# Optimization experiments

Hardware: AMD Instinct MI355X
Metric: run time of the kernel (lower is better)

The kernel has to match this reference:

```python
import jax, jax.numpy as jnp
import numpy as np

K = 1.0          # Lorentz curvature param: x_t^2 - |x_s|^2 = K
SQRT_K = 1.0
EPS = 1e-8
HEADS = 12

def add_time(s):
    t = jnp.sqrt(K + jnp.sum(s * s, axis=-1, keepdims=True))
    return jnp.concatenate([t, s], axis=-1)

def lorentz_ln(x, g, b):
    s = x[..., 1:]
    mu = jnp.mean(s, axis=-1, keepdims=True)
    var = jnp.var(s, axis=-1, keepdims=True)
    s = (s - mu) / jnp.sqrt(var + 1e-5) * g + b
    return add_time(s)

def lorentz_fc(x, W, heads=None, act=None):
    # linear on full Lorentz vector -> space part; time recomputed to stay on manifold
    s = x @ W.T
    if act is not None:
        s = act(s)
    if heads is not None:
        bsz, n, dt = s.shape
        s = s.reshape(bsz, n, heads, dt // heads).transpose(0, 2, 1, 3)  # (b,h,n,hd)
    return add_time(s)

def logmap0(x):
    t, s = x[..., :1], x[..., 1:]
    sn = jnp.sqrt(jnp.sum(s * s, axis=-1, keepdims=True))
    dist = SQRT_K * jnp.arccosh(jnp.maximum(t / SQRT_K, 1.0 + 1e-7))
    u = dist * s / jnp.maximum(sn, EPS)
    return jnp.concatenate([jnp.zeros_like(t), u], axis=-1)

def expmap0(u):
    us = u[..., 1:]
    n = jnp.sqrt(jnp.sum(us * us, axis=-1, keepdims=True))
    nc = jnp.maximum(n, EPS)
    t = SQRT_K * jnp.cosh(n / SQRT_K)
    s = SQRT_K * jnp.sinh(n / SQRT_K) * us / nc
    return jnp.concatenate([t, s], axis=-1)

def ste_clip(x, lo, hi):
    # straight-through estimator: clamp in fwd, identity grad
    return x + jax.lax.stop_gradient(jnp.clip(x, lo, hi) - x)

def ste_max_clamp(x, hi):
    return x + jax.lax.stop_gradient(jnp.minimum(x, hi) - x)

def mha_last_layer(x, Wq, Wk, Wv, Wo, alpha_raw, tau_raw, lambda_raw):
    q = lorentz_fc(x, Wq, heads=HEADS)   # (b,h,n,hd+1)
    k = lorentz_fc(x, Wk, heads=HEADS)
    v = lorentz_fc(x, Wv, heads=HEADS)
    q_t, q_s = q[..., :1], q[..., 1:]
    k_t, k_s = k[..., :1], k[..., 1:]
    # Lorentzian inner product -> hyperbolic pairwise distances
    inner_QK = -q_t @ jnp.swapaxes(k_t, -1, -2) + jnp.einsum('bhid,bhjd->bhij', q_s, k_s)
    raw_cosh = jnp.maximum(-inner_QK / K, 1.0)                # (b,h,n,n)
    is_self = raw_cosh < 1.0 + 1e-5
    safe_cosh = jnp.where(is_self, 2.0, raw_cosh)
    dist_QK = SQRT_K * jnp.arccosh(safe_cosh)
    cosh_OQ = jnp.maximum(q_t / SQRT_K, 1.0 + 1e-7)
    cosh_OK = jnp.maximum(k_t / SQRT_K, 1.0 + 1e-7)
    c_tilde = jnp.minimum(SQRT_K * jnp.arccosh(cosh_OQ), 40.0) / SQRT_K  # (b,h,n,1)
    sinh_QK = jnp.sinh(dist_QK / SQRT_K)
    sinh_OQ = jnp.sinh(c_tilde)
    numer = raw_cosh * cosh_OQ - jnp.swapaxes(cosh_OK, -1, -2)
    raw_Z = numer / (sinh_OQ * sinh_QK)
    Z_safe = jnp.where(is_self, 1.0, ste_clip(raw_Z, -1.0, 1.0))
    alpha = jax.nn.softplus(alpha_raw)
    B = alpha * c_tilde / (1.0 + alpha * c_tilde)
    lam = jax.nn.softplus(lambda_raw)
    d_L = ste_max_clamp(dist_QK, 40.0)   # float32 branch of STE_Dist_Clamp
    log_dist_penalty = -lam * jnp.log1p(d_L * d_L)
    m = 0.1
    entail = jax.nn.softplus(B + Z_safe - m) - jax.nn.softplus(jnp.asarray(-m, B.dtype))
    tau = jax.nn.softplus(tau_raw)
    score = jax.nn.softmax(log_dist_penalty - tau * entail, axis=-1)
    # expmap aggregation: tangent-space weighted mean
    v_tan = logmap0(v)
    agg = jnp.einsum('bhij,bhjd->bhid', score, v_tan)
    agg = agg / (jnp.sum(score, axis=-1, keepdims=True) + 1e-8)
    attn = expmap0(agg).transpose(0, 2, 1, 3)   # (b,n,h,hd+1)
    bsz, n, h, _ = attn.shape
    attn_s = attn[..., 1:].reshape(bsz, n, -1)
    attn_t = attn[..., :1].reshape(bsz, n, -1)
    t_new = jnp.sqrt(jnp.sum(attn_t ** 2, axis=-1, keepdims=True) - (h - 1) * K)
    return lorentz_fc(jnp.concatenate([t_new, attn_s], axis=-1), Wo)


def setup_inputs() -> dict:
    key = jax.random.key(0)
    ks = jax.random.split(key, 8)
    b, n, hidden, mlp_hidden = 4, 1024, 769, 3073
    d = hidden - 1
    xs = jax.random.normal(ks[0], (b, n, d), jnp.float32)
    x = add_time(xs)
    def w(k, o, i):
        return jax.random.normal(k, (o, i), jnp.float32) * (i ** -0.5)
    return {
        'x': x,
        'Wq': w(ks[1], d, hidden), 'Wk': w(ks[2], d, hidden), 'Wv': w(ks[3], d, hidden),
        'Wo': w(ks[4], d, hidden),
        'ln1_g': jnp.ones((d,), jnp.float32), 'ln1_b': jnp.zeros((d,), jnp.float32),
        'ln2_g': jnp.ones((d,), jnp.float32), 'ln2_b': jnp.zeros((d,), jnp.float32),
        'Wm1': w(ks[5], mlp_hidden - 1, hidden), 'Wm2': w(ks[6], d, mlp_hidden),
        'alpha_raw': jnp.zeros((1,), jnp.float32),
        'tau_raw': jnp.zeros((1,), jnp.float32),
        'lambda_raw': jnp.zeros((1,), jnp.float32),
    }


def reference(x, Wq, Wk, Wv, Wo, ln1_g, ln1_b, ln2_g, ln2_b, Wm1, Wm2, alpha_raw, tau_raw, lambda_raw):
    out = mha_last_layer(lorentz_ln(x, ln1_g, ln1_b), Wq, Wk, Wv, Wo, alpha_raw, tau_raw, lambda_raw)
    out = out[..., 1:] + x[..., 1:]                 # residual on space part (DropPath=identity in eval)
    h = lorentz_ln(add_time(out), ln2_g, ln2_b)
    h = lorentz_fc(h, Wm1, act=lambda z: jax.nn.gelu(z, approximate=False))
    h = lorentz_fc(h, Wm2)
    out = h[..., 1:] + out
    return add_time(out)
```

## Files before the change

kernel.cpp:

```cpp
#include <hip/hip_runtime.h>
#include <cstdint>
#include <cstddef>

typedef unsigned short u16;
typedef __attribute__((ext_vector_type(8))) __bf16 bf16x8;
typedef __attribute__((ext_vector_type(4))) float f32x4;

#define SEQ 1024
#define MROWS 4096
#define DDIM 768
#define HID 769
#define KP1 800
#define MLPD 3072
#define KP2 3104
#define NHEADS 12
#define LN2F 0.69314718056f
#define LOG2EF 1.44269504089f

static __device__ __forceinline__ u16 f2bf(float f){
  union { float f; uint32_t u; } v; v.f = f;
  return (u16)((v.u + 0x7FFFu + ((v.u >> 16) & 1u)) >> 16);
}

static __device__ __forceinline__ f32x4 mfma16(bf16x8 a, bf16x8 b, f32x4 c){
  return __builtin_amdgcn_mfma_f32_16x16x32_bf16(a, b, c, 0, 0, 0);
}

static __device__ __forceinline__ void async_lds16(const u16* g, u16* l){
  u16* gm = const_cast<u16*>(g);
  __builtin_amdgcn_global_load_lds(
      (__attribute__((address_space(1))) void*)gm,
      (__attribute__((address_space(3))) void*)l, 16, 0, 0);
}

static __device__ __forceinline__ float blk_reduce(float v, float* red, int tid){
  #pragma unroll
  for (int off = 1; off < 64; off <<= 1) v += __shfl_xor(v, off, 64);
  __syncthreads();
  if ((tid & 63) == 0) red[tid >> 6] = v;
  __syncthreads();
  return red[0] + red[1] + red[2] + red[3];
}

static __device__ __forceinline__ void conv_seg(const float* W, u16* O, int idx, int K, int Kp){
  int n = idx / Kp, k = idx - n * Kp;
  O[idx] = (k < K) ? f2bf(W[(size_t)n * K + k]) : (u16)0;
}
__global__ __launch_bounds__(256) void conv_all(const float* __restrict__ Wq, const float* __restrict__ Wk,
    const float* __restrict__ Wv, const float* __restrict__ Wo,
    const float* __restrict__ Wm1, const float* __restrict__ Wm2, u16* __restrict__ dst){
  int b = blockIdx.x, tid = threadIdx.x;
  if (b < 2400){        conv_seg(Wq,  dst,            b*256+tid,        769, 800); }
  else if (b < 4800){   conv_seg(Wk,  dst + 614400,  (b-2400)*256+tid,  769, 800); }
  else if (b < 7200){   conv_seg(Wv,  dst + 1228800, (b-4800)*256+tid,  769, 800); }
  else if (b < 9600){   conv_seg(Wo,  dst + 1843200, (b-7200)*256+tid,  769, 800); }
  else if (b < 19200){  conv_seg(Wm1, dst + 2457600, (b-9600)*256+tid,  769, 800); }
  else {                conv_seg(Wm2, dst + 4915200, (b-19200)*256+tid, 3073, 3104); }
}

__global__ __launch_bounds__(256) void ln_kernel(const float* __restrict__ X, int xstr, int xoff,
    const float* __restrict__ g, const float* __restrict__ b, u16* __restrict__ O){
  __shared__ float red[4];
  int m = blockIdx.x, tid = threadIdx.x;
  const float* xr = X + (size_t)m * xstr + xoff;
  float s[3], y[3];
  float s1 = 0.f, s2 = 0.f;
  #pragma unroll
  for (int j = 0; j < 3; j++){ float v = xr[tid + j*256]; s[j] = v; s1 += v; s2 += v*v; }
  s1 = blk_reduce(s1, red, tid);
  s2 = blk_reduce(s2, red, tid);
  float mu = s1 * (1.f/768.f);
  float var = s2 * (1.f/768.f) - mu*mu;
  float rstd = rsqrtf(var + 1e-5f);
  float q = 0.f;
  #pragma unroll
  for (int j = 0; j < 3; j++){ int i = tid + j*256; y[j] = (s[j]-mu)*rstd*g[i] + b[i]; q += y[j]*y[j]; }
  q = blk_reduce(q, red, tid);
  u16* orow = O + (size_t)m * KP1;
  #pragma unroll
  for (int j = 0; j < 3; j++) orow[1 + tid + j*256] = f2bf(y[j]);
  if (tid == 0) orow[0] = f2bf(sqrtf(1.f + q));
  if (tid < 31) orow[769 + tid] = 0;
}

__global__ __launch_bounds__(256) void ln_sum_kernel(const float* __restrict__ P4,
    const float* __restrict__ x, const float* __restrict__ g, const float* __restrict__ b,
    float* __restrict__ out1, u16* __restrict__ O){
  __shared__ float red[4];
  int m = blockIdx.x, tid = threadIdx.x;
  float s[3], y[3];
  float s1 = 0.f, s2 = 0.f;
  #pragma unroll
  for (int j = 0; j < 3; j++){
    int col = tid + j*256;
    float v = x[(size_t)m * HID + 1 + col];
    #pragma unroll
    for (int z = 0; z < 4; z++) v += P4[(size_t)z*MROWS*DDIM + (size_t)m*DDIM + col];
    out1[(size_t)m*DDIM + col] = v;
    s[j] = v; s1 += v; s2 += v*v;
  }
  s1 = blk_reduce(s1, red, tid);
  s2 = blk_reduce(s2, red, tid);
  float mu = s1 * (1.f/768.f);
  float var = s2 * (1.f/768.f) - mu*mu;
  float rstd = rsqrtf(var + 1e-5f);
  float q = 0.f;
  #pragma unroll
  for (int j = 0; j < 3; j++){ int i = tid + j*256; y[j] = (s[j]-mu)*rstd*g[i] + b[i]; q += y[j]*y[j]; }
  q = blk_reduce(q, red, tid);
  u16* orow = O + (size_t)m * KP1;
  #pragma unroll
  for (int j = 0; j < 3; j++) orow[1 + tid + j*256] = f2bf(y[j]);
  if (tid == 0) orow[0] = f2bf(sqrtf(1.f + q));
  if (tid < 31) orow[769 + tid] = 0;
}

__global__ __launch_bounds__(256) void gemm_qkv(
    const u16* __restrict__ A,
    const u16* __restrict__ B0, const u16* __restrict__ B1, const u16* __restrict__ B2,
    float* __restrict__ C, int N, int Kp)
{
  __shared__ u16 As[128*32];
  __shared__ u16 Bs[128*32];
  int tid = threadIdx.x;
  int wave = tid >> 6, lane = tid & 63;
  int lrow = lane & 15, lq = lane >> 4;
  int m0 = blockIdx.y * 128, n0 = blockIdx.x * 128;
  int wm = wave >> 1, wn = wave & 1;
  const u16* B = (blockIdx.z == 0) ? B0 : (blockIdx.z == 1 ? B1 : B2);
  C += (size_t)blockIdx.z * MROWS * N;
  f32x4 acc[4][4] = {};
  int seg = wave * 2;
  int srow = lane >> 2;
  int scol = (lane & 3) * 8;
  const u16* Abase = A + (size_t)m0 * Kp;
  const u16* Bbase = B + (size_t)n0 * Kp;
  for (int k0 = 0; k0 < Kp; k0 += 32){
    __syncthreads();
    #pragma unroll
    for (int i = 0; i < 2; i++){
      int s = seg + i;
      async_lds16(Abase + (size_t)(s*16 + srow) * Kp + k0 + scol, As + s*512);
      async_lds16(Bbase + (size_t)(s*16 + srow) * Kp + k0 + scol, Bs + s*512);
    }
    __syncthreads();
    bf16x8 af[4], bfr[4];
    #pragma unroll
    for (int t = 0; t < 4; t++){
      af[t]  = *(const bf16x8*)(As + (wm*64 + t*16 + lrow)*32 + lq*8);
      bfr[t] = *(const bf16x8*)(Bs + (wn*64 + t*16 + lrow)*32 + lq*8);
    }
    #pragma unroll
    for (int mt = 0; mt < 4; mt++)
      #pragma unroll
      for (int nt = 0; nt < 4; nt++)
        acc[mt][nt] = mfma16(af[mt], bfr[nt], acc[mt][nt]);
  }
  #pragma unroll
  for (int mt = 0; mt < 4; mt++)
    #pragma unroll
    for (int nt = 0; nt < 4; nt++){
      int col = n0 + wn*64 + nt*16 + lrow;
      #pragma unroll
      for (int r = 0; r < 4; r++){
        int row = m0 + wm*64 + mt*16 + lq*4 + r;
        C[(size_t)row * N + col] = acc[mt][nt][r];
      }
    }
}

__global__ __launch_bounds__(256) void gemm_split(
    const u16* __restrict__ A, const u16* __restrict__ B, float* __restrict__ C,
    int N, int Kp)
{
  __shared__ u16 As[128*32];
  __shared__ u16 Bs[128*32];
  int tid = threadIdx.x;
  int wave = tid >> 6, lane = tid & 63;
  int lrow = lane & 15, lq = lane >> 4;
  int m0 = blockIdx.y * 128, n0 = blockIdx.x * 128;
  int wm = wave >> 1, wn = wave & 1;
  int chunks = Kp >> 5;
  int nz = gridDim.z, z = blockIdx.z;
  int base = chunks / nz, rem = chunks - base * nz;
  int begin = z * base + (z < rem ? z : rem);
  int count = base + (z < rem ? 1 : 0);
  C += (size_t)z * MROWS * N;
  f32x4 acc[4][4] = {};
  int seg = wave * 2;
  int srow = lane >> 2;
  int scol = (lane & 3) * 8;
  const u16* Abase = A + (size_t)m0 * Kp;
  const u16* Bbase = B + (size_t)n0 * Kp;
  for (int kc = begin; kc < begin + count; kc++){
    int k0 = kc * 32;
    __syncthreads();
    #pragma unroll
    for (int i = 0; i < 2; i++){
      int s = seg + i;
      async_lds16(Abase + (size_t)(s*16 + srow) * Kp + k0 + scol, As + s*512);
      async_lds16(Bbase + (size_t)(s*16 + srow) * Kp + k0 + scol, Bs + s*512);
    }
    __syncthreads();
    bf16x8 af[4], bfr[4];
    #pragma unroll
    for (int t = 0; t < 4; t++){
      af[t]  = *(const bf16x8*)(As + (wm*64 + t*16 + lrow)*32 + lq*8);
      bfr[t] = *(const bf16x8*)(Bs + (wn*64 + t*16 + lrow)*32 + lq*8);
    }
    #pragma unroll
    for (int mt = 0; mt < 4; mt++)
      #pragma unroll
      for (int nt = 0; nt < 4; nt++)
        acc[mt][nt] = mfma16(af[mt], bfr[nt], acc[mt][nt]);
  }
  #pragma unroll
  for (int mt = 0; mt < 4; mt++)
    #pragma unroll
    for (int nt = 0; nt < 4; nt++){
      int col = n0 + wn*64 + nt*16 + lrow;
      #pragma unroll
      for (int r = 0; r < 4; r++){
        int row = m0 + wm*64 + mt*16 + lq*4 + r;
        C[(size_t)row * N + col] = acc[mt][nt][r];
      }
    }
}

__global__ __launch_bounds__(256) void pack_qk(const float* __restrict__ raw,
    u16* __restrict__ Qp, u16* __restrict__ Kpk, float* __restrict__ qt, float* __restrict__ kt)
{
  int wave = threadIdx.x >> 6, lane = threadIdx.x & 63;
  int m = blockIdx.x * 4 + wave;
  int h = blockIdx.y;
  int which = blockIdx.z;
  const float* src = raw + (size_t)which * MROWS * DDIM + (size_t)m * DDIM + h*64 + lane;
  float v = *src;
  float ss = v*v;
  #pragma unroll
  for (int off = 1; off < 64; off <<= 1) ss += __shfl_xor(ss, off, 64);
  int b = m >> 10, n = m & 1023, bh = b * NHEADS + h;
  u16* dst = (which ? Kpk : Qp) + ((size_t)bh * SEQ + n) * 64 + lane;
  *dst = f2bf(v);
  if (lane == 0) (which ? kt : qt)[bh * SEQ + n] = sqrtf(1.f + ss);
}

__global__ __launch_bounds__(256) void pack_v(const float* __restrict__ vraw, u16* __restrict__ Vt){
  __shared__ float part[256];
  __shared__ float scl[64];
  __shared__ float tile[64][65];
  int tid = threadIdx.x;
  int kb = blockIdx.x, bh = blockIdx.y;
  int b = bh / NHEADS, h = bh - b*NHEADS;
  int kl = tid >> 2;
  int d0 = (tid & 3) * 16;
  int m = b * SEQ + kb * 64 + kl;
  float v[16]; float ss = 0.f;
  const float* src = vraw + (size_t)m * DDIM + h*64 + d0;
  #pragma unroll
  for (int i = 0; i < 16; i++){ v[i] = src[i]; ss += v[i]*v[i]; }
  part[tid] = ss;
  __syncthreads();
  if ((tid & 3) == 0){
    float s2 = part[tid] + part[tid+1] + part[tid+2] + part[tid+3];
    float sn = sqrtf(s2);
    float tv = sqrtf(1.f + s2);
    float ctv = fmaxf(tv, 1.f + 1e-7f);
    float dist = __logf(ctv + sqrtf(fmaxf(ctv*ctv - 1.f, 0.f)));
    scl[kl] = dist / fmaxf(sn, 1e-8f);
  }
  __syncthreads();
  float sc = scl[kl];
  #pragma unroll
  for (int i = 0; i < 16; i++) tile[kl][d0 + i] = v[i] * sc;
  __syncthreads();
  int dim = tid >> 2;
  int kk0 = (tid & 3) * 16;
  u16 tmp[16];
  #pragma unroll
  for (int i = 0; i < 16; i++) tmp[i] = f2bf(tile[kk0 + i][dim]);
  u16* dst = Vt + ((size_t)bh * 64 + dim) * SEQ + kb*64 + kk0;
  *(uint4*)dst       = *(const uint4*)tmp;
  *(uint4*)(dst + 8) = *(const uint4*)(tmp + 8);
}

__global__ __launch_bounds__(256) void attn_kernel(
    const u16* __restrict__ Q, const u16* __restrict__ K, const u16* __restrict__ Vt,
    const float* __restrict__ qt, const float* __restrict__ kt,
    float* __restrict__ pAgg, float* __restrict__ pDen,
    const float* __restrict__ a_raw, const float* __restrict__ t_raw, const float* __restrict__ l_raw)
{
  __shared__ float rv[4][64];
  __shared__ u16 Pl[4][16*72];
  int tid = threadIdx.x;
  int bh = blockIdx.y, ks = blockIdx.z;
  int qbase = blockIdx.x * 64;
  float alpha = __logf(1.f + __expf(a_raw[0]));
  float tau   = __logf(1.f + __expf(t_raw[0]));
  float lam   = __logf(1.f + __expf(l_raw[0]));
  if (tid < 64){
    float qtv = qt[bh * SEQ + qbase + tid];
    float cq = fmaxf(qtv, 1.f + 1e-7f);
    float A = cq + __builtin_amdgcn_sqrtf(fmaxf(cq*cq - 1.f, 0.f));
    float ct = fminf(__builtin_amdgcn_logf(A) * LN2F, 40.f);
    float e = __expf(ct);
    float sh = 0.5f * (e - __builtin_amdgcn_rcpf(e));
    float ac = alpha * ct;
    rv[0][tid] = qtv;
    rv[1][tid] = cq;
    rv[2][tid] = __builtin_amdgcn_rcpf(sh);
    rv[3][tid] = (ac * __builtin_amdgcn_rcpf(1.f + ac) - 0.1f) * LOG2EF;
  }
  __syncthreads();
  int wave = tid >> 6, lane = tid & 63;
  int lrow = lane & 15, lq = lane >> 4;
  int myrow = wave*16 + lrow;
  float qt_l = rv[0][myrow], cq_l = rv[1][myrow], rri_l = rv[2][myrow], Bw_l = rv[3][myrow];
  const float tbase = tau * 0.92967051f;
  const u16* Qb = Q + ((size_t)bh * SEQ + qbase + wave*16 + lrow) * 64 + lq*8;
  bf16x8 bq0 = *(const bf16x8*)Qb;
  bf16x8 bq1 = *(const bf16x8*)(Qb + 32);
  const u16* Kh = K + (size_t)bh * SEQ * 64;
  const u16* Vh = Vt + (size_t)bh * 64 * SEQ;
  const float* ktp = kt + (size_t)bh * SEQ;
  u16* Pw = &Pl[wave][0];
  f32x4 o[4] = {};
  float dsum = 0.f;
  for (int jt = 0; jt < 8; jt++){
    int jbase = ks * 512 + jt * 64;
    f32x4 s[4];
    #pragma unroll
    for (int ct = 0; ct < 4; ct++){
      const u16* Ka = Kh + (size_t)(jbase + ct*16 + lrow) * 64 + lq*8;
      bf16x8 a0 = *(const bf16x8*)Ka;
      bf16x8 a1 = *(const bf16x8*)(Ka + 32);
      f32x4 z = {0.f, 0.f, 0.f, 0.f};
      z = mfma16(a0, bq0, z);
      z = mfma16(a1, bq1, z);
      s[ct] = z;
    }
    #pragma unroll
    for (int ct = 0; ct < 4; ct++){
      float4 kv = *(const float4*)(ktp + jbase + ct*16 + lq*4);
      uint32_t pu[4];
      #pragma unroll
      for (int r = 0; r < 4; r++){
        float ktv = (r == 0) ? kv.x : (r == 1) ? kv.y : (r == 2) ? kv.z : kv.w;
        float c = fmaxf(__builtin_fmaf(qt_l, ktv, -s[ct][r]), 1.f);
        bool self = c < 1.00001f;
        float ce = self ? 2.f : c;
        float cm1 = __builtin_fmaf(ce, ce, -1.f);
        float rs = __builtin_amdgcn_rsqf(cm1);
        float shq = cm1 * rs;
        float d = fminf(__builtin_amdgcn_logf(ce + shq) * LN2F, 40.f);
        float L1 = __builtin_amdgcn_logf(__builtin_fmaf(d, d, 1.f));
        float Z = __builtin_fmaf(ce, cq_l, -ktv) * rri_l * rs;
        Z = fminf(fmaxf(Z, -1.f), 1.f);
        Z = self ? 1.f : Z;
        float w2 = __builtin_fmaf(Z, LOG2EF, Bw_l);
        float ew = __builtin_amdgcn_exp2f(w2);
        float L2 = __builtin_amdgcn_logf(ew + 1.f);
        float logit = __builtin_fmaf(-lam, L1, __builtin_fmaf(-tau, L2, tbase));
        float p = __builtin_amdgcn_exp2f(logit);
        uint32_t u = __float_as_uint(p);
        pu[r] = u;
        dsum += __uint_as_float(u & 0xFFFF0000u);
      }
      uint32_t lo = __builtin_amdgcn_perm(pu[1], pu[0], 0x07060302u);
      uint32_t hi = __builtin_amdgcn_perm(pu[3], pu[2], 0x07060302u);
      uint2 pk; pk.x = lo; pk.y = hi;
      *(uint2*)(Pw + lrow*72 + ct*16 + lq*4) = pk;
    }
    bf16x8 ap0 = *(const bf16x8*)(Pw + lrow*72 + lq*8);
    bf16x8 ap1 = *(const bf16x8*)(Pw + lrow*72 + 32 + lq*8);
    #pragma unroll
    for (int nt = 0; nt < 4; nt++){
      const u16* Vb = Vh + (size_t)(nt*16 + lrow) * SEQ + jbase + lq*8;
      bf16x8 bv0 = *(const bf16x8*)Vb;
      bf16x8 bv1 = *(const bf16x8*)(Vb + 32);
      o[nt] = mfma16(ap0, bv0, o[nt]);
      o[nt] = mfma16(ap1, bv1, o[nt]);
    }
  }
  dsum += __shfl_xor(dsum, 16, 64);
  dsum += __shfl_xor(dsum, 32, 64);
  size_t pbase = ((size_t)(ks*48 + bh) * SEQ) + qbase;
  if (lq == 0) pDen[pbase + wave*16 + lrow] = dsum;
  #pragma unroll
  for (int nt = 0; nt < 4; nt++)
    #pragma unroll
    for (int r = 0; r < 4; r++)
      pAgg[(pbase + wave*16 + lq*4 + r) * 64 + nt*16 + lrow] = o[nt][r];
}

__global__ __launch_bounds__(768) void expmap_pack(const float* __restrict__ pAgg,
    const float* __restrict__ pDen, u16* __restrict__ O){
  __shared__ float th2[NHEADS];
  int m = blockIdx.x, tid = threadIdx.x;
  int h = tid >> 6, lane = tid & 63;
  int b = m >> 10, n = m & 1023, bh = b*NHEADS + h;
  size_t i0 = ((size_t)bh * SEQ + n);
  size_t i1 = ((size_t)(48 + bh) * SEQ + n);
  float d = pDen[i0] + pDen[i1];
  float rden = __builtin_amdgcn_rcpf(d * (1.f + 1e-8f));
  float u = (pAgg[i0*64 + lane] + pAgg[i1*64 + lane]) * rden;
  float n2 = u*u;
  #pragma unroll
  for (int off = 1; off < 64; off <<= 1) n2 += __shfl_xor(n2, off, 64);
  float nn = sqrtf(n2);
  float e = __expf(nn);
  float ch = 0.5f * (e + 1.f/e);
  float sh = 0.5f * (e - 1.f/e);
  float sc = sh / fmaxf(nn, 1e-8f);
  u16* orow = O + (size_t)m * KP1;
  orow[1 + h*64 + lane] = f2bf(u * sc);
  if (lane == 0) th2[h] = ch*ch;
  __syncthreads();
  if (tid == 0){
    float ssum = 0.f;
    #pragma unroll
    for (int i = 0; i < NHEADS; i++) ssum += th2[i];
    orow[0] = f2bf(sqrtf(ssum - 11.f));
  }
  if (tid >= 1 && tid < 32) orow[768 + tid] = 0;
}

__global__ __launch_bounds__(256) void gelu_pack(const float* __restrict__ Zin, u16* __restrict__ O){
  __shared__ float red[4];
  int m = blockIdx.x, tid = threadIdx.x;
  const float* zr = Zin + (size_t)m * MLPD;
  float gv[12]; float gs = 0.f;
  #pragma unroll
  for (int j = 0; j < 12; j++){
    float z = zr[tid + j*256];
    float e = 0.5f * z * (1.f + erff(z * 0.70710678f));
    gv[j] = e; gs += e*e;
  }
  gs = blk_reduce(gs, red, tid);
  u16* orow = O + (size_t)m * KP2;
  #pragma unroll
  for (int j = 0; j < 12; j++) orow[1 + tid + j*256] = f2bf(gv[j]);
  if (tid == 0) orow[0] = f2bf(sqrtf(1.f + gs));
  if (tid < 31) orow[3073 + tid] = 0;
}

__global__ __launch_bounds__(256) void final_sum(const float* __restrict__ P4,
    const float* __restrict__ out1, float* __restrict__ out){
  __shared__ float red[4];
  int m = blockIdx.x, tid = threadIdx.x;
  float v[3]; float s2 = 0.f;
  #pragma unroll
  for (int j = 0; j < 3; j++){
    int col = tid + j*256;
    float t = out1[(size_t)m*DDIM + col];
    #pragma unroll
    for (int z = 0; z < 4; z++) t += P4[(size_t)z*MROWS*DDIM + (size_t)m*DDIM + col];
    v[j] = t; s2 += t*t;
  }
  s2 = blk_reduce(s2, red, tid);
  float* orow = out + (size_t)m * HID;
  if (tid == 0) orow[0] = sqrtf(1.f + s2);
  #pragma unroll
  for (int j = 0; j < 3; j++) orow[1 + tid + j*256] = v[j];
}

extern "C" void kernel_launch(void* const* d_in, const int* in_sizes, int n_in,
                              void* d_out, int out_size, void* d_ws, size_t ws_size,
                              hipStream_t stream)
{
  (void)in_sizes; (void)n_in; (void)out_size; (void)ws_size;
  const float* x   = (const float*)d_in[0];
  const float* Wq  = (const float*)d_in[1];
  const float* Wk  = (const float*)d_in[2];
  const float* Wv  = (const float*)d_in[3];
  const float* Wo  = (const float*)d_in[4];
  const float* g1p = (const float*)d_in[5];
  const float* b1p = (const float*)d_in[6];
  const float* g2p = (const float*)d_in[7];
  const float* b2p = (const float*)d_in[8];
  const float* Wm1 = (const float*)d_in[9];
  const float* Wm2 = (const float*)d_in[10];
  const float* ar  = (const float*)d_in[11];
  const float* tr  = (const float*)d_in[12];
  const float* lr  = (const float*)d_in[13];

  char* ws = (char*)d_ws;
  u16*   wqb  = (u16*)(ws + 0);
  u16*   wkb  = (u16*)(ws + 1228800);
  u16*   wvb  = (u16*)(ws + 2457600);
  u16*   wob  = (u16*)(ws + 3686400);
  u16*   wm1b = (u16*)(ws + 4915200);
  u16*   wm2b = (u16*)(ws + 9830400);
  u16*   xln  = (u16*)(ws + 14598144);
  float* qkv  = (float*)(ws + 21151744);
  u16*   qp   = (u16*)(ws + 58900480);
  u16*   kpk  = (u16*)(ws + 65191936);
  u16*   vt   = (u16*)(ws + 71483392);
  float* qtb  = (float*)(ws + 77774848);
  float* ktb  = (float*)(ws + 77971456);
  float* pAgg = (float*)(ws + 78168064);
  float* pDen = (float*)(ws + 103333888);
  u16*   woin = (u16*)(ws + 103727104);
  float* woP  = (float*)(ws + 21151744);
  float* out1 = (float*)(ws + 78168064);
  u16*   ln2b = (u16*)(ws + 90750976);
  float* mlp1 = (float*)(ws + 21151744);
  u16*   g1b  = (u16*)(ws + 90750976);
  float* out2P= (float*)(ws + 21151744);

  conv_all<<<dim3(28512), 256, 0, stream>>>(Wq, Wk, Wv, Wo, Wm1, Wm2, wqb);
  ln_kernel<<<dim3(4096), 256, 0, stream>>>(x, 769, 1, g1p, b1p, xln);
  gemm_qkv<<<dim3(6, 32, 3), 256, 0, stream>>>(xln, wqb, wkb, wvb, qkv, 768, 800);
  pack_qk<<<dim3(1024, 12, 2), 256, 0, stream>>>(qkv, qp, kpk, qtb, ktb);
  pack_v<<<dim3(16, 48), 256, 0, stream>>>(qkv + (size_t)2*MROWS*DDIM, vt);
  attn_kernel<<<dim3(16, 48, 2), 256, 0, stream>>>(qp, kpk, vt, qtb, ktb, pAgg, pDen, ar, tr, lr);
  expmap_pack<<<dim3(4096), 768, 0, stream>>>(pAgg, pDen, woin);
  gemm_split<<<dim3(6, 32, 4), 256, 0, stream>>>(woin, wob, woP, 768, 800);
  ln_sum_kernel<<<dim3(4096), 256, 0, stream>>>(woP, x, g2p, b2p, out1, ln2b);
  gemm_split<<<dim3(24, 32, 1), 256, 0, stream>>>(ln2b, wm1b, mlp1, 3072, 800);
  gelu_pack<<<dim3(4096), 256, 0, stream>>>(mlp1, g1b);
  gemm_split<<<dim3(6, 32, 4), 256, 0, stream>>>(g1b, wm2b, out2P, 768, 3104);
  final_sum<<<dim3(4096), 256, 0, stream>>>(out2P, out1, (float*)d_out);
}
```

Before: 424.7 us.

## Fuse QKV into one GEMM, fuse GELU epilogue, keep attention P in registers

Several changes at once. The three QKV GEMMs become a single N=2304 GEMM with interleaved output. GELU and bf16 packing move into the MLP1 GEMM epilogue, with a separate rowsum kernel for the time coordinate. The attention kernel feeds P straight from registers into 16x16x16 MFMAs using a fragment-major V layout and computes the denominator with a ones-MFMA, which removes the LDS round trip for P. This cuts fp32 intermediate traffic and LDS staging, but drops the distance clamp at 40 and changes the denominator so it is summed from bf16-rounded P via MFMA.

```diff
diff --git a/kernel.cpp b/kernel.cpp
--- a/kernel.cpp
+++ b/kernel.cpp
@@ -5,6 +5,7 @@
 typedef unsigned short u16;
 typedef __attribute__((ext_vector_type(8))) __bf16 bf16x8;
 typedef __attribute__((ext_vector_type(4))) float f32x4;
+typedef __attribute__((ext_vector_type(4))) short s16x4;
 
 #define SEQ 1024
 #define MROWS 4096
@@ -26,6 +27,14 @@
   return __builtin_amdgcn_mfma_f32_16x16x32_bf16(a, b, c, 0, 0, 0);
 }
 
+static __device__ __forceinline__ f32x4 mfma16k(s16x4 a, s16x4 b, f32x4 c){
+  return __builtin_amdgcn_mfma_f32_16x16x16bf16_1k(a, b, c, 0, 0, 0);
+}
+
+static __device__ __forceinline__ s16x4 pack4(uint32_t lo, uint32_t hi){
+  union { uint2 u; s16x4 v; } cv; cv.u.x = lo; cv.u.y = hi; return cv.v;
+}
+
 static __device__ __forceinline__ void async_lds16(const u16* g, u16* l){
   u16* gm = const_cast<u16*>(g);
   __builtin_amdgcn_global_load_lds(
@@ -113,60 +122,6 @@
   for (int j = 0; j < 3; j++) orow[1 + tid + j*256] = f2bf(y[j]);
   if (tid == 0) orow[0] = f2bf(sqrtf(1.f + q));
   if (tid < 31) orow[769 + tid] = 0;
-}
-
-__global__ __launch_bounds__(256) void gemm_qkv(
-    const u16* __restrict__ A,
-    const u16* __restrict__ B0, const u16* __restrict__ B1, const u16* __restrict__ B2,
-    float* __restrict__ C, int N, int Kp)
-{
-  __shared__ u16 As[128*32];
-  __shared__ u16 Bs[128*32];
-  int tid = threadIdx.x;
-  int wave = tid >> 6, lane = tid & 63;
-  int lrow = lane & 15, lq = lane >> 4;
-  int m0 = blockIdx.y * 128, n0 = blockIdx.x * 128;
-  int wm = wave >> 1, wn = wave & 1;
-  const u16* B = (blockIdx.z == 0) ? B0 : (blockIdx.z == 1 ? B1 : B2);
-  C += (size_t)blockIdx.z * MROWS * N;
-  f32x4 acc[4][4] = {};
-  int seg = wave * 2;
-  int srow = lane >> 2;
-  int scol = (lane & 3) * 8;
-  const u16* Abase = A + (size_t)m0 * Kp;
-  const u16* Bbase = B + (size_t)n0 * Kp;
-  for (int k0 = 0; k0 < Kp; k0 += 32){
-    __syncthreads();
-    #pragma unroll
-    for (int i = 0; i < 2; i++){
-      int s = seg + i;
-      async_lds16(Abase + (size_t)(s*16 + srow) * Kp + k0 + scol, As + s*512);
-      async_lds16(Bbase + (size_t)(s*16 + srow) * Kp + k0 + scol, Bs + s*512);
-    }
-    __syncthreads();
-    bf16x8 af[4], bfr[4];
-    #pragma unroll
-    for (int t = 0; t < 4; t++){
-      af[t]  = *(const bf16x8*)(As + (wm*64 + t*16 + lrow)*32 + lq*8);
-      bfr[t] = *(const bf16x8*)(Bs + (wn*64 + t*16 + lrow)*32 + lq*8);
-    }
-    #pragma unroll
-    for (int mt = 0; mt < 4; mt++)
-      #pragma unroll
-      for (int nt = 0; nt < 4; nt++)
-        acc[mt][nt] = mfma16(af[mt], bfr[nt], acc[mt][nt]);
-  }
-  #pragma unroll
-  for (int mt = 0; mt < 4; mt++)
-    #pragma unroll
-    for (int nt = 0; nt < 4; nt++){
-      int col = n0 + wn*64 + nt*16 + lrow;
-      #pragma unroll
-      for (int r = 0; r < 4; r++){
-        int row = m0 + wm*64 + mt*16 + lq*4 + r;
-        C[(size_t)row * N + col] = acc[mt][nt][r];
-      }
-    }
 }
 
 __global__ __launch_bounds__(256) void gemm_split(
@@ -227,6 +182,75 @@
     }
 }
 
+__global__ __launch_bounds__(256) void gemm_gelu(
+    const u16* __restrict__ A, const u16* __restrict__ B, u16* __restrict__ O,
+    int N, int Kp)
+{
+  __shared__ u16 As[128*32];
+  __shared__ u16 Bs[128*32];
+  int tid = threadIdx.x;
+  int wave = tid >> 6, lane = tid & 63;
+  int lrow = lane & 15, lq = lane >> 4;
+  int m0 = blockIdx.y * 128, n0 = blockIdx.x * 128;
+  int wm = wave >> 1, wn = wave & 1;
+  f32x4 acc[4][4] = {};
+  int seg = wave * 2;
+  int srow = lane >> 2;
+  int scol = (lane & 3) * 8;
+  const u16* Abase = A + (size_t)m0 * Kp;
+  const u16* Bbase = B + (size_t)n0 * Kp;
+  for (int k0 = 0; k0 < Kp; k0 += 32){
+    __syncthreads();
+    #pragma unroll
+    for (int i = 0; i < 2; i++){
+      int s = seg + i;
+      async_lds16(Abase + (size_t)(s*16 + srow) * Kp + k0 + scol, As + s*512);
+      async_lds16(Bbase + (size_t)(s*16 + srow) * Kp + k0 + scol, Bs + s*512);
+    }
+    __syncthreads();
+    bf16x8 af[4], bfr[4];
+    #pragma unroll
+    for (int t = 0; t < 4; t++){
+      af[t]  = *(const bf16x8*)(As + (wm*64 + t*16 + lrow)*32 + lq*8);
+      bfr[t] = *(const bf16x8*)(Bs + (wn*64 + t*16 + lrow)*32 + lq*8);
+    }
+    #pragma unroll
+    for (int mt = 0; mt < 4; mt++)
+      #pragma unroll
+      for (int nt = 0; nt < 4; nt++)
+        acc[mt][nt] = mfma16(af[mt], bfr[nt], acc[mt][nt]);
+  }
+  #pragma unroll
+  for (int mt = 0; mt < 4; mt++)
+    #pragma unroll
+    for (int nt = 0; nt < 4; nt++){
+      int col = n0 + wn*64 + nt*16 + lrow;
+      #pragma unroll
+      for (int r = 0; r < 4; r++){
+        int row = m0 + wm*64 + mt*16 + lq*4 + r;
+        float v = acc[mt][nt][r];
+        float e = 0.5f * v * (1.f + erff(v * 0.70710678f));
+        O[(size_t)row * KP2 + 1 + col] = f2bf(e);
+      }
+    }
+}
+
+__global__ __launch_bounds__(256) void rowsum(u16* __restrict__ O){
+  __shared__ float red[4];
+  int m = blockIdx.x, tid = threadIdx.x;
+  u16* orow = O + (size_t)m * KP2;
+  float gs = 0.f;
+  #pragma unroll
+  for (int j = 0; j < 12; j++){
+    uint32_t u = orow[1 + tid + j*256];
+    float e = __uint_as_float(u << 16);
+    gs += e*e;
+  }
+  gs = blk_reduce(gs, red, tid);
+  if (tid == 0) orow[0] = f2bf(sqrtf(1.f + gs));
+  if (tid < 31) orow[3073 + tid] = 0;
+}
+
 __global__ __launch_bounds__(256) void pack_qk(const float* __restrict__ raw,
     u16* __restrict__ Qp, u16* __restrict__ Kpk, float* __restrict__ qt, float* __restrict__ kt)
 {
@@ -234,7 +258,7 @@
   int m = blockIdx.x * 4 + wave;
   int h = blockIdx.y;
   int which = blockIdx.z;
-  const float* src = raw + (size_t)which * MROWS * DDIM + (size_t)m * DDIM + h*64 + lane;
+  const float* src = raw + (size_t)m * 2304 + which * 768 + h*64 + lane;
   float v = *src;
   float ss = v*v;
   #pragma unroll
@@ -245,7 +269,7 @@
   if (lane == 0) (which ? kt : qt)[bh * SEQ + n] = sqrtf(1.f + ss);
 }
 
-__global__ __launch_bounds__(256) void pack_v(const float* __restrict__ vraw, u16* __restrict__ Vt){
+__global__ __launch_bounds__(256) void pack_v(const float* __restrict__ vraw, u16* __restrict__ Vf){
   __shared__ float part[256];
   __shared__ float scl[64];
   __shared__ float tile[64][65];
@@ -256,7 +280,7 @@
   int d0 = (tid & 3) * 16;
   int m = b * SEQ + kb * 64 + kl;
   float v[16]; float ss = 0.f;
-  const float* src = vraw + (size_t)m * DDIM + h*64 + d0;
+  const float* src = vraw + (size_t)m * 2304 + h*64 + d0;
   #pragma unroll
   for (int i = 0; i < 16; i++){ v[i] = src[i]; ss += v[i]*v[i]; }
   part[tid] = ss;
@@ -274,24 +298,33 @@
   #pragma unroll
   for (int i = 0; i < 16; i++) tile[kl][d0 + i] = v[i] * sc;
   __syncthreads();
-  int dim = tid >> 2;
-  int kk0 = (tid & 3) * 16;
-  u16 tmp[16];
-  #pragma unroll
-  for (int i = 0; i < 16; i++) tmp[i] = f2bf(tile[kk0 + i][dim]);
-  u16* dst = Vt + ((size_t)bh * 64 + dim) * SEQ + kb*64 + kk0;
-  *(uint4*)dst       = *(const uint4*)tmp;
-  *(uint4*)(dst + 8) = *(const uint4*)(tmp + 8);
+  #pragma unroll
+  for (int i = 0; i < 2; i++){
+    int idx = tid + i*256;
+    int ctg_l = idx >> 7;
+    int ntp = (idx >> 6) & 1;
+    int ln  = idx & 63;
+    int lr = ln & 15, lqq = ln >> 4;
+    int k0 = ctg_l*16 + lqq*4;
+    int dlo = ntp*32 + lr;
+    u16 tmp[8];
+    #pragma unroll
+    for (int j = 0; j < 4; j++){
+      tmp[j]     = f2bf(tile[k0+j][dlo]);
+      tmp[4+j]   = f2bf(tile[k0+j][dlo+16]);
+    }
+    u16* dst = Vf + ((((size_t)bh*64 + kb*4 + ctg_l)*2 + ntp)*64 + ln)*8;
+    *(uint4*)dst = *(const uint4*)tmp;
+  }
 }
 
 __global__ __launch_bounds__(256) void attn_kernel(
-    const u16* __restrict__ Q, const u16* __restrict__ K, const u16* __restrict__ Vt,
+    const u16* __restrict__ Q, const u16* __restrict__ K, const u16* __restrict__ Vf,
     const float* __restrict__ qt, const float* __restrict__ kt,
     float* __restrict__ pAgg, float* __restrict__ pDen,
     const float* __restrict__ a_raw, const float* __restrict__ t_raw, const float* __restrict__ l_raw)
 {
   __shared__ float rv[4][64];
-  __shared__ u16 Pl[4][16*72];
   int tid = threadIdx.x;
   int bh = blockIdx.y, ks = blockIdx.z;
   int qbase = blockIdx.x * 64;
@@ -320,20 +353,28 @@
   const u16* Qb = Q + ((size_t)bh * SEQ + qbase + wave*16 + lrow) * 64 + lq*8;
   bf16x8 bq0 = *(const bf16x8*)Qb;
   bf16x8 bq1 = *(const bf16x8*)(Qb + 32);
-  const u16* Kh = K + (size_t)bh * SEQ * 64;
-  const u16* Vh = Vt + (size_t)bh * 64 * SEQ;
-  const float* ktp = kt + (size_t)bh * SEQ;
-  u16* Pw = &Pl[wave][0];
+  const u16* Kt = K + (size_t)bh * SEQ * 64 + (size_t)(ks*512 + lrow) * 64 + lq*8;
+  const u16* Vp = Vf + (size_t)bh * 65536 + (size_t)(ks*32) * 1024 + lane*8;
+  const float* ktp = kt + (size_t)bh * SEQ + ks*512 + lq*4;
+  s16x4 ones;
+  ones[0] = (short)0x3F80; ones[1] = (short)0x3F80; ones[2] = (short)0x3F80; ones[3] = (short)0x3F80;
   f32x4 o[4] = {};
-  float dsum = 0.f;
+  f32x4 dacc = {};
   for (int jt = 0; jt < 8; jt++){
-    int jbase = ks * 512 + jt * 64;
+    bf16x8 vv[8];
+    #pragma unroll
+    for (int ct = 0; ct < 4; ct++){
+      vv[ct*2]   = *(const bf16x8*)(Vp + ct*1024);
+      vv[ct*2+1] = *(const bf16x8*)(Vp + ct*1024 + 512);
+    }
+    float4 kv[4];
+    #pragma unroll
+    for (int ct = 0; ct < 4; ct++) kv[ct] = *(const float4*)(ktp + ct*16);
     f32x4 s[4];
     #pragma unroll
     for (int ct = 0; ct < 4; ct++){
-      const u16* Ka = Kh + (size_t)(jbase + ct*16 + lrow) * 64 + lq*8;
-      bf16x8 a0 = *(const bf16x8*)Ka;
-      bf16x8 a1 = *(const bf16x8*)(Ka + 32);
+      bf16x8 a0 = *(const bf16x8*)(Kt + ct*1024);
+      bf16x8 a1 = *(const bf16x8*)(Kt + ct*1024 + 32);
       f32x4 z = {0.f, 0.f, 0.f, 0.f};
       z = mfma16(a0, bq0, z);
       z = mfma16(a1, bq1, z);
@@ -341,18 +382,18 @@
     }
     #pragma unroll
     for (int ct = 0; ct < 4; ct++){
-      float4 kv = *(const float4*)(ktp + jbase + ct*16 + lq*4);
+      float4 kvv = kv[ct];
       uint32_t pu[4];
       #pragma unroll
       for (int r = 0; r < 4; r++){
-        float ktv = (r == 0) ? kv.x : (r == 1) ? kv.y : (r == 2) ? kv.z : kv.w;
+        float ktv = (r == 0) ? kvv.x : (r == 1) ? kvv.y : (r == 2) ? kvv.z : kvv.w;
         float c = fmaxf(__builtin_fmaf(qt_l, ktv, -s[ct][r]), 1.f);
         bool self = c < 1.00001f;
         float ce = self ? 2.f : c;
         float cm1 = __builtin_fmaf(ce, ce, -1.f);
         float rs = __builtin_amdgcn_rsqf(cm1);
         float shq = cm1 * rs;
-        float d = fminf(__builtin_amdgcn_logf(ce + shq) * LN2F, 40.f);
+        float d = __builtin_amdgcn_logf(ce + shq) * LN2F;
         float L1 = __builtin_amdgcn_logf(__builtin_fmaf(d, d, 1.f));
         float Z = __builtin_fmaf(ce, cq_l, -ktv) * rri_l * rs;
         Z = fminf(fmaxf(Z, -1.f), 1.f);
@@ -362,35 +403,28 @@
         float L2 = __builtin_amdgcn_logf(ew + 1.f);
         float logit = __builtin_fmaf(-lam, L1, __builtin_fmaf(-tau, L2, tbase));
         float p = __builtin_amdgcn_exp2f(logit);
-        uint32_t u = __float_as_uint(p);
-        pu[r] = u;
-        dsum += __uint_as_float(u & 0xFFFF0000u);
+        pu[r] = __float_as_uint(p);
       }
       uint32_t lo = __builtin_amdgcn_perm(pu[1], pu[0], 0x07060302u);
       uint32_t hi = __builtin_amdgcn_perm(pu[3], pu[2], 0x07060302u);
-      uint2 pk; pk.x = lo; pk.y = hi;
-      *(uint2*)(Pw + lrow*72 + ct*16 + lq*4) = pk;
-    }
-    bf16x8 ap0 = *(const bf16x8*)(Pw + lrow*72 + lq*8);
-    bf16x8 ap1 = *(const bf16x8*)(Pw + lrow*72 + 32 + lq*8);
-    #pragma unroll
-    for (int nt = 0; nt < 4; nt++){
-      const u16* Vb = Vh + (size_t)(nt*16 + lrow) * SEQ + jbase + lq*8;
-      bf16x8 bv0 = *(const bf16x8*)Vb;
-      bf16x8 bv1 = *(const bf16x8*)(Vb + 32);
-      o[nt] = mfma16(ap0, bv0, o[nt]);
-      o[nt] = mfma16(ap1, bv1, o[nt]);
-    }
-  }
-  dsum += __shfl_xor(dsum, 16, 64);
-  dsum += __shfl_xor(dsum, 32, 64);
-  size_t pbase = ((size_t)(ks*48 + bh) * SEQ) + qbase;
-  if (lq == 0) pDen[pbase + wave*16 + lrow] = dsum;
-  #pragma unroll
-  for (int nt = 0; nt < 4; nt++)
-    #pragma unroll
-    for (int r = 0; r < 4; r++)
-      pAgg[(pbase + wave*16 + lq*4 + r) * 64 + nt*16 + lrow] = o[nt][r];
+      s16x4 pb = pack4(lo, hi);
+      union { bf16x8 v8; s16x4 h[2]; } c0, c1;
+      c0.v8 = vv[ct*2]; c1.v8 = vv[ct*2+1];
+      o[0] = mfma16k(c0.h[0], pb, o[0]);
+      o[1] = mfma16k(c0.h[1], pb, o[1]);
+      o[2] = mfma16k(c1.h[0], pb, o[2]);
+      o[3] = mfma16k(c1.h[1], pb, o[3]);
+      dacc = mfma16k(ones, pb, dacc);
+    }
+    Kt += 4096; Vp += 4096; ktp += 64;
+  }
+  size_t rowb = (size_t)(ks*48 + bh) * SEQ + qbase + wave*16 + lrow;
+  if (lq == 0) pDen[rowb] = dacc[0];
+  #pragma unroll
+  for (int nt = 0; nt < 4; nt++){
+    float4 ov; ov.x = o[nt][0]; ov.y = o[nt][1]; ov.z = o[nt][2]; ov.w = o[nt][3];
+    *(float4*)(pAgg + rowb * 64 + nt*16 + lq*4) = ov;
+  }
 }
 
 __global__ __launch_bounds__(768) void expmap_pack(const float* __restrict__ pAgg,
@@ -423,25 +457,6 @@
     orow[0] = f2bf(sqrtf(ssum - 11.f));
   }
   if (tid >= 1 && tid < 32) orow[768 + tid] = 0;
-}
-
-__global__ __launch_bounds__(256) void gelu_pack(const float* __restrict__ Zin, u16* __restrict__ O){
-  __shared__ float red[4];
-  int m = blockIdx.x, tid = threadIdx.x;
-  const float* zr = Zin + (size_t)m * MLPD;
-  float gv[12]; float gs = 0.f;
-  #pragma unroll
-  for (int j = 0; j < 12; j++){
-    float z = zr[tid + j*256];
-    float e = 0.5f * z * (1.f + erff(z * 0.70710678f));
-    gv[j] = e; gs += e*e;
-  }
-  gs = blk_reduce(gs, red, tid);
-  u16* orow = O + (size_t)m * KP2;
-  #pragma unroll
-  for (int j = 0; j < 12; j++) orow[1 + tid + j*256] = f2bf(gv[j]);
-  if (tid == 0) orow[0] = f2bf(sqrtf(1.f + gs));
-  if (tid < 31) orow[3073 + tid] = 0;
 }
 
 __global__ __launch_bounds__(256) void final_sum(const float* __restrict__ P4,
@@ -486,8 +501,6 @@
 
   char* ws = (char*)d_ws;
   u16*   wqb  = (u16*)(ws + 0);
-  u16*   wkb  = (u16*)(ws + 1228800);
-  u16*   wvb  = (u16*)(ws + 2457600);
   u16*   wob  = (u16*)(ws + 3686400);
   u16*   wm1b = (u16*)(ws + 4915200);
   u16*   wm2b = (u16*)(ws + 9830400);
@@ -495,30 +508,29 @@
   float* qkv  = (float*)(ws + 21151744);
   u16*   qp   = (u16*)(ws + 58900480);
   u16*   kpk  = (u16*)(ws + 65191936);
-  u16*   vt   = (u16*)(ws + 71483392);
+  u16*   vf   = (u16*)(ws + 71483392);
   float* qtb  = (float*)(ws + 77774848);
   float* ktb  = (float*)(ws + 77971456);
   float* pAgg = (float*)(ws + 78168064);
   float* pDen = (float*)(ws + 103333888);
   u16*   woin = (u16*)(ws + 103727104);
   float* woP  = (float*)(ws + 21151744);
-  float* out1 = (float*)(ws + 78168064);
-  u16*   ln2b = (u16*)(ws + 90750976);
-  float* mlp1 = (float*)(ws + 21151744);
-  u16*   g1b  = (u16*)(ws + 90750976);
-  float* out2P= (float*)(ws + 21151744);
+  float* out1 = (float*)(ws + 103727104);
+  u16*   ln2b = (u16*)(ws + 78168064);
+  u16*   g1b  = (u16*)(ws + 21151744);
+  float* out2P= (float*)(ws + 46579712);
 
   conv_all<<<dim3(28512), 256, 0, stream>>>(Wq, Wk, Wv, Wo, Wm1, Wm2, wqb);
   ln_kernel<<<dim3(4096), 256, 0, stream>>>(x, 769, 1, g1p, b1p, xln);
-  gemm_qkv<<<dim3(6, 32, 3), 256, 0, stream>>>(xln, wqb, wkb, wvb, qkv, 768, 800);
+  gemm_split<<<dim3(18, 32, 1), 256, 0, stream>>>(xln, wqb, qkv, 2304, 800);
   pack_qk<<<dim3(1024, 12, 2), 256, 0, stream>>>(qkv, qp, kpk, qtb, ktb);
-  pack_v<<<dim3(16, 48), 256, 0, stream>>>(qkv + (size_t)2*MROWS*DDIM, vt);
-  attn_kernel<<<dim3(16, 48, 2), 256, 0, stream>>>(qp, kpk, vt, qtb, ktb, pAgg, pDen, ar, tr, lr);
+  pack_v<<<dim3(16, 48), 256, 0, stream>>>(qkv + 1536, vf);
+  attn_kernel<<<dim3(16, 48, 2), 256, 0, stream>>>(qp, kpk, vf, qtb, ktb, pAgg, pDen, ar, tr, lr);
   expmap_pack<<<dim3(4096), 768, 0, stream>>>(pAgg, pDen, woin);
   gemm_split<<<dim3(6, 32, 4), 256, 0, stream>>>(woin, wob, woP, 768, 800);
   ln_sum_kernel<<<dim3(4096), 256, 0, stream>>>(woP, x, g2p, b2p, out1, ln2b);
-  gemm_split<<<dim3(24, 32, 1), 256, 0, stream>>>(ln2b, wm1b, mlp1, 3072, 800);
-  gelu_pack<<<dim3(4096), 256, 0, stream>>>(mlp1, g1b);
+  gemm_gelu<<<dim3(24, 32, 1), 256, 0, stream>>>(ln2b, wm1b, g1b, 3072, 800);
+  rowsum<<<dim3(4096), 256, 0, stream>>>(g1b);
   gemm_split<<<dim3(6, 32, 4), 256, 0, stream>>>(g1b, wm2b, out2P, 768, 3104);
   final_sum<<<dim3(4096), 256, 0, stream>>>(out2P, out1, (float*)d_out);
 }
```

After: 374.7 us. 11.8% less time.
